# Performance work log

Hardware: AMD Instinct MI355X
Metric: run time of the kernel (lower is better)

The kernel has to match this reference:

```python
import jax, jax.numpy as jnp
import numpy as np

F_DIM, H, B, MAX = 128, 256, 256, 128
N = B * MAX            # 32768 nodes, 256 graphs of 128 nodes each
E = 524288             # avg degree 16
EPS = 1e-5


def _bn(x, g, b):
    # BatchNorm1d in training mode: biased batch stats over the node axis
    m = x.mean(0)
    v = x.var(0)
    return (x - m) * jax.lax.rsqrt(v + EPS) * g + b


def _gcn(x, W, b, src, dst, n):
    # PyG GCNConv: add self-loops, symmetric deg^-1/2 normalization
    h = x @ W
    loops = jnp.arange(n, dtype=src.dtype)
    s = jnp.concatenate([src, loops])
    d = jnp.concatenate([dst, loops])
    deg = jax.ops.segment_sum(jnp.ones_like(s, dtype=x.dtype), d, num_segments=n)
    dinv = jax.lax.rsqrt(jnp.maximum(deg, 1.0))
    norm = dinv[s] * dinv[d]
    out = jax.ops.segment_sum(h[s] * norm[:, None], d, num_segments=n)
    return out + b


def setup_inputs() -> dict:
    key = jax.random.key(0)
    ks = jax.random.split(key, 20)

    def xavier(k, shape, gain=1.414):
        lim = gain * np.sqrt(6.0 / (shape[0] + shape[1]))
        return jax.random.uniform(k, shape, jnp.float32, -lim, lim)

    inp = {}
    inp['x'] = jax.random.normal(ks[0], (N, F_DIM), jnp.float32)
    inp['src_local'] = jax.random.randint(ks[1], (E,), 0, MAX, jnp.int32)
    inp['dst_local'] = jax.random.randint(ks[2], (E,), 0, MAX, jnp.int32)
    dims = [(F_DIM, H), (H, H), (H, H)]
    for i, (di, do) in enumerate(dims):
        inp[f'gcn_w{i}'] = xavier(ks[3 + i], (di, do))
        inp[f'gcn_b{i}'] = jnp.zeros((do,), jnp.float32)
        inp[f'bn_g{i}'] = jnp.ones((do,), jnp.float32)
        inp[f'bn_b{i}'] = jnp.zeros((do,), jnp.float32)
    inp['sc_w0'] = xavier(ks[6], (F_DIM, H), 1.0)
    inp['sc_b0'] = jnp.zeros((H,), jnp.float32)
    inp['edge_w'] = xavier(ks[7], (H, H), 0.01)
    inp['fd_w0'] = xavier(ks[8], (H, H)); inp['fd_b0'] = jnp.zeros((H,), jnp.float32)
    inp['fd_g0'] = jnp.ones((H,), jnp.float32); inp['fd_be0'] = jnp.zeros((H,), jnp.float32)
    inp['fd_w1'] = xavier(ks[9], (H, H)); inp['fd_b1'] = jnp.zeros((H,), jnp.float32)
    inp['fd_g1'] = jnp.ones((H,), jnp.float32); inp['fd_be1'] = jnp.zeros((H,), jnp.float32)
    inp['fd_w2'] = xavier(ks[10], (H, F_DIM)); inp['fd_b2'] = jnp.zeros((F_DIM,), jnp.float32)
    inp['ph_w0'] = xavier(ks[11], (H, H)); inp['ph_b0'] = jnp.zeros((H,), jnp.float32)
    inp['ph_w1'] = xavier(ks[12], (H, H)); inp['ph_b1'] = jnp.zeros((H,), jnp.float32)
    return inp


def reference(x, src_local, dst_local,
              gcn_w0, gcn_b0, bn_g0, bn_b0, sc_w0, sc_b0,
              gcn_w1, gcn_b1, bn_g1, bn_b1,
              gcn_w2, gcn_b2, bn_g2, bn_b2,
              edge_w,
              fd_w0, fd_b0, fd_g0, fd_be0,
              fd_w1, fd_b1, fd_g1, fd_be1,
              fd_w2, fd_b2,
              ph_w0, ph_b0, ph_w1, ph_b1):
    n = x.shape[0]
    # global edge index: edge e belongs to graph e // (E//B); offset by g*MAX
    off = (jnp.arange(E, dtype=jnp.int32) // (E // B)) * MAX
    src = src_local + off
    dst = dst_local + off

    def block(h, W, b, g, bb, shortcut):
        res = shortcut(h)
        out = jax.nn.relu(_bn(_gcn(h, W, b, src, dst, n), g, bb))
        return jax.nn.relu(out + res)  # dropout is identity at inference

    z = block(x, gcn_w0, gcn_b0, bn_g0, bn_b0, lambda h: h @ sc_w0 + sc_b0)
    z = block(z, gcn_w1, gcn_b1, bn_g1, bn_b1, lambda h: h)
    z = block(z, gcn_w2, gcn_b2, bn_g2, bn_b2, lambda h: h)
    # F.normalize(p=2, dim=1)
    z = z / jnp.maximum(jnp.linalg.norm(z, axis=1, keepdims=True), 1e-12)

    # BilinearEdgeDecoder per graph, vectorized: sigmoid(Z W Z^T) with zero diag
    zb = z.reshape(B, MAX, H)
    adj = jax.nn.sigmoid(jnp.einsum('bnd,de,bme->bnm', zb, edge_w, zb))
    adj = adj * (1.0 - jnp.eye(MAX, dtype=adj.dtype))

    # Feature_Decoder: [Linear,ReLU,BN] x2 then Linear
    h = _bn(jax.nn.relu(z @ fd_w0 + fd_b0), fd_g0, fd_be0)
    h = _bn(jax.nn.relu(h @ fd_w1 + fd_b1), fd_g1, fd_be1)
    x_recon = h @ fd_w2 + fd_b2

    z_g = zb.max(axis=1)  # global_max_pool per graph
    z_g_mlp = jax.nn.relu(z_g @ ph_w0 + ph_b0) @ ph_w1 + ph_b1
    return (z, adj, x_recon, z_g, z_g_mlp)
```

## Files before the change

### kernel.cpp

```cpp
#include <hip/hip_runtime.h>
#include <hip/hip_bf16.h>

using bf = __hip_bfloat16;
typedef __attribute__((ext_vector_type(8))) short s8;
typedef __attribute__((ext_vector_type(4))) float f4;

constexpr int NN  = 32768;
constexpr int HD  = 256;

__device__ __forceinline__ float u2f(unsigned short h) {
    union { unsigned u; float f; } x; x.u = ((unsigned)h) << 16;
    return x.f;
}
__device__ __forceinline__ unsigned short f2u(float f) {
    union { float f; unsigned u; } x; x.f = f;
    unsigned r = x.u + 0x7FFF + ((x.u >> 16) & 1);
    return (unsigned short)(r >> 16);
}
__device__ __forceinline__ bf f2bf(float f) {
    unsigned short h = f2u(f);
    return *reinterpret_cast<bf*>(&h);
}
__device__ __forceinline__ float bf2f(bf b) {
    return u2f(*reinterpret_cast<unsigned short*>(&b));
}

__device__ __forceinline__ int swz(int row, int slot) {
    return row * 64 + ((slot ^ (row & 7)) << 3);
}
__device__ __forceinline__ int swz128(int row, int slot) {
    return row * 128 + ((slot ^ (row & 7)) << 3);
}

typedef const __attribute__((address_space(1))) unsigned int guint;
typedef __attribute__((address_space(3))) unsigned int luint;
__device__ __forceinline__ void gload16(const void* g, void* l) {
    __builtin_amdgcn_global_load_lds((guint*)g, (luint*)l, 16, 0, 0);
}

struct WTd { const float* src; int K, N, off; };
struct WTpack { WTd w[10]; };

__global__ __launch_bounds__(256) void k_prep(const int* __restrict__ srcL,
                                              const int* __restrict__ dstL,
                                              const float* __restrict__ xf,
                                              WTpack p, bf* __restrict__ A,
                                              bf* __restrict__ xb,
                                              bf* __restrict__ wT) {
    __shared__ __align__(16) float shm[8320];
    int b = blockIdx.x, t = threadIdx.x;
    if (b < 256) {
        float* sT = shm;
        float* sdin = shm + 8192;
        int g = b;
        const int* sg = srcL + (g << 11);
        const int* dg = dstL + (g << 11);
        if (t < 128) sdin[t] = 0.f;
        __syncthreads();
        for (int e = t; e < 2048; e += 256) atomicAdd(&sdin[dg[e]], 1.0f);
        __syncthreads();
        if (t < 128) sdin[t] = rsqrtf(sdin[t] + 1.0f);
        __syncthreads();
        bf* out = A + ((long)g << 14);
        for (int half = 0; half < 2; ++half) {
            for (int i = t; i < 8192; i += 256) sT[i] = 0.f;
            __syncthreads();
            for (int e = t; e < 2048; e += 256) {
                int s = sg[e], d = dg[e];
                if ((s >> 6) == half)
                    atomicAdd(&sT[(d << 6) + (s & 63)], sdin[s] * sdin[d]);
            }
            __syncthreads();
            if (t < 128 && (t >> 6) == half)
                sT[(t << 6) + (t & 63)] += sdin[t] * sdin[t];
            __syncthreads();
            for (int i4 = t; i4 < 2048; i4 += 256) {
                int d = i4 >> 4, c4 = (i4 & 15) * 4;
                float4 v = *(float4*)&sT[(d << 6) + c4];
                ushort4 u = make_ushort4(f2u(v.x), f2u(v.y), f2u(v.z), f2u(v.w));
                *(ushort4*)&out[(d << 7) + (half << 6) + c4] = u;
            }
            __syncthreads();
        }
    } else if (b < 416) {
        int idx = b - 256;
        WTd d = p.w[idx >> 4];
        int rem = idx & 15;
        int n0 = (rem & 3) * 64, k0 = (rem >> 2) * 64;
        if (n0 >= d.N || k0 >= d.K) return;
        float (*s)[65] = (float(*)[65])shm;
        int cc = t & 63, rq = t >> 6;
#pragma unroll
        for (int i = 0; i < 16; ++i) {
            int r = i * 4 + rq;
            s[r][cc] = d.src[(long)(k0 + r) * d.N + n0 + cc];
        }
        __syncthreads();
#pragma unroll
        for (int i = 0; i < 16; ++i) {
            int r = i * 4 + rq;
            wT[d.off + (long)(n0 + r) * d.K + k0 + cc] = f2bf(s[cc][r]);
        }
    } else {
        long base = (long)(b - 416) * 16384;
#pragma unroll
        for (int it = 0; it < 16; ++it) {
            long i4 = base + (it * 256 + t) * 4;
            float4 v = *(const float4*)&xf[i4];
            *(ushort4*)&xb[i4] = make_ushort4(f2u(v.x), f2u(v.y), f2u(v.z), f2u(v.w));
        }
    }
}

__device__ __forceinline__ void mfma_s1(const bf* sA, const bf* sB, f4 (&acc)[4][2],
                                        int wm, int wn, int l15, int kq) {
#pragma unroll
    for (int ks = 0; ks < 2; ++ks) {
        s8 af[4], bg[2];
#pragma unroll
        for (int f = 0; f < 4; ++f)
            af[f] = *(const s8*)&sA[swz(wm * 64 + f * 16 + l15, kq + 4 * ks)];
#pragma unroll
        for (int f = 0; f < 2; ++f)
            bg[f] = *(const s8*)&sB[swz(wn * 32 + f * 16 + l15, kq + 4 * ks)];
#pragma unroll
        for (int fr = 0; fr < 4; ++fr)
#pragma unroll
            for (int fc = 0; fc < 2; ++fc)
                acc[fr][fc] = __builtin_amdgcn_mfma_f32_16x16x32_bf16(
                    af[fr], bg[fc], acc[fr][fc], 0, 0, 0);
    }
}

__device__ __forceinline__ void mfma_s2(const bf* sA, const bf* sB, f4 (&acc)[4][2],
                                        int wm, int wn, int l15, int kq) {
#pragma unroll
    for (int ks = 0; ks < 4; ++ks) {
        s8 af[4], bg[2];
#pragma unroll
        for (int f = 0; f < 4; ++f)
            af[f] = *(const s8*)&sA[swz128(wm * 64 + f * 16 + l15, ks * 4 + kq)];
#pragma unroll
        for (int f = 0; f < 2; ++f)
            bg[f] = *(const s8*)&sB[swz128(wn * 32 + f * 16 + l15, ks * 4 + kq)];
#pragma unroll
        for (int fr = 0; fr < 4; ++fr)
#pragma unroll
            for (int fc = 0; fc < 2; ++fc)
                acc[fr][fc] = __builtin_amdgcn_mfma_f32_16x16x32_bf16(
                    af[fr], bg[fc], acc[fr][fc], 0, 0, 0);
    }
}

__device__ __forceinline__ void tstore(bf* sOut, f4 (&acc)[4][2],
                                       int wm, int wn, int l15, int kq) {
#pragma unroll
    for (int fr = 0; fr < 4; ++fr) {
        int rl = wm * 64 + fr * 16 + kq * 4;
#pragma unroll
        for (int fc = 0; fc < 2; ++fc) {
            int cl = wn * 32 + fc * 16 + l15;
            ushort4 q = make_ushort4(f2u(acc[fr][fc][0]), f2u(acc[fr][fc][1]),
                                     f2u(acc[fr][fc][2]), f2u(acc[fr][fc][3]));
            int off = cl * 128 + (((rl >> 3) ^ (cl & 7)) << 3) + (rl & 7);
            *(ushort4*)&sOut[off] = q;
        }
    }
}

template <int MODE>
__global__ __launch_bounds__(512) void k_fused(
    const bf* __restrict__ Xin,
    const bf* __restrict__ Res, const float* __restrict__ stats,
    const bf* __restrict__ Wt, const bf* __restrict__ Wt2,
    const float* __restrict__ scb, const bf* __restrict__ Adj,
    bf* __restrict__ Zout, bf* __restrict__ AG, bf* __restrict__ ResOut,
    float* __restrict__ part) {
    __shared__ __align__(16) bf sOut[16384];
    __shared__ __align__(16) bf sStg[16384];
    const int g = blockIdx.x;
    const int h = blockIdx.y;
    const int t = threadIdx.x;
    const int lane = t & 63, w = t >> 6;
    const int wm = w >> 2, wn = w & 3;
    const int l15 = lane & 15, kq = lane >> 4;
    constexpr int KS1 = (MODE == 2) ? 128 : 256;
    const bf* Xg = Xin + (long)g * ((MODE == 2) ? 16384 : 32768);
    const bf* Rg = (MODE == 0) ? Res + (long)g * 32768 : nullptr;

    f4 acc1[4][2] = {};
    for (int k0 = 0; k0 < KS1; k0 += 64) {
        __syncthreads();
#pragma unroll
        for (int i = 0; i < 2; ++i) {
            if constexpr (MODE == 0) {
                int sdx = i * 512 + t;
                int row = sdx >> 3, sl = sdx & 7;
                int c = k0 + sl * 8;
                s8 av = *(const s8*)&Xg[row * 256 + c];
                s8 rv = *(const s8*)&Rg[row * 256 + c];
                float4 sc0 = *(const float4*)&stats[c];
                float4 sc1 = *(const float4*)&stats[c + 4];
                float4 sh0 = *(const float4*)&stats[256 + c];
                float4 sh1 = *(const float4*)&stats[256 + c + 4];
                float scv[8] = {sc0.x, sc0.y, sc0.z, sc0.w, sc1.x, sc1.y, sc1.z, sc1.w};
                float shv[8] = {sh0.x, sh0.y, sh0.z, sh0.w, sh1.x, sh1.y, sh1.z, sh1.w};
                unsigned short* u = (unsigned short*)&av;
                const unsigned short* ru = (const unsigned short*)&rv;
#pragma unroll
                for (int j = 0; j < 8; ++j) {
                    float v = fmaf(u2f(u[j]), scv[j], shv[j]);
                    v = fmaxf(v, 0.f) + u2f(ru[j]);
                    u[j] = f2u(fmaxf(v, 0.f));
                }
                if (h == 0)
                    *(s8*)&Zout[(long)g * 32768 + row * 256 + c] = av;
                *(s8*)&sStg[swz(row, sl)] = av;
            } else {
                int r0 = i * 64 + 8 * w;
                int rw = r0 + (lane >> 3);
                int ps = ((lane & 7) ^ (rw & 7)) << 3;
                gload16(&Xg[rw * 128 + k0 + ps], &sStg[r0 * 64]);
            }
            {
                int r0 = i * 64 + 8 * w;
                int rw = r0 + (lane >> 3);
                int ps = ((lane & 7) ^ (rw & 7)) << 3;
                const bf* bsrc;
                if constexpr (MODE == 0)
                    bsrc = &Wt[(h * 128 + rw) * 256 + k0 + ps];
                else {
                    const bf* Wsrc = (h < 2) ? Wt : Wt2;
                    bsrc = &Wsrc[((h & 1) * 128 + rw) * 128 + k0 + ps];
                }
                gload16(bsrc, &sStg[8192 + r0 * 64]);
            }
        }
        __syncthreads();
        mfma_s1(sStg, sStg + 8192, acc1, wm, wn, l15, kq);
    }
    if (MODE == 2 && h >= 2) {
#pragma unroll
        for (int fr = 0; fr < 4; ++fr) {
            int rl = wm * 64 + fr * 16 + kq * 4;
#pragma unroll
            for (int fc = 0; fc < 2; ++fc) {
                int cl = wn * 32 + fc * 16 + l15;
                float bv = scb[(h - 2) * 128 + cl];
#pragma unroll
                for (int i = 0; i < 4; ++i)
                    ResOut[(long)(g * 128 + rl + i) * 256 + (h - 2) * 128 + cl] =
                        f2bf(acc1[fr][fc][i] + bv);
            }
        }
        return;
    }
    tstore(sOut, acc1, wm, wn, l15, kq);
    __syncthreads();
#pragma unroll
    for (int i = 0; i < 4; ++i) {
        int r0 = i * 32 + 4 * w;
        int rw = r0 + (lane >> 4);
        int ps = ((lane & 15) ^ (rw & 7)) << 3;
        gload16(&Adj[((long)g << 14) + rw * 128 + ps], &sStg[r0 * 128]);
    }
    __syncthreads();
    f4 acc2[4][2] = {};
    mfma_s2(sStg, sOut, acc2, wm, wn, l15, kq);
    float ps[2] = {0.f, 0.f}, ps2[2] = {0.f, 0.f};
#pragma unroll
    for (int fr = 0; fr < 4; ++fr) {
        int rl = wm * 64 + fr * 16 + kq * 4;
#pragma unroll
        for (int fc = 0; fc < 2; ++fc) {
            int cl = wn * 32 + fc * 16 + l15;
#pragma unroll
            for (int i = 0; i < 4; ++i) {
                float v = acc2[fr][fc][i];
                ps[fc] += v; ps2[fc] += v * v;
                AG[(long)(g * 128 + rl + i) * 256 + (h & 1) * 128 + cl] = f2bf(v);
            }
        }
    }
    __syncthreads();
    float* scr = (float*)sStg;
#pragma unroll
    for (int fc = 0; fc < 2; ++fc) {
        ps[fc] += __shfl_xor(ps[fc], 16);  ps[fc] += __shfl_xor(ps[fc], 32);
        ps2[fc] += __shfl_xor(ps2[fc], 16); ps2[fc] += __shfl_xor(ps2[fc], 32);
    }
    if (lane < 16) {
#pragma unroll
        for (int fc = 0; fc < 2; ++fc) {
            int c = wn * 32 + fc * 16 + lane;
            scr[(c * 2 + wm) * 2 + 0] = ps[fc];
            scr[(c * 2 + wm) * 2 + 1] = ps2[fc];
        }
    }
    __syncthreads();
    if (t < 256) {
        int col = t & 127, s = t >> 7;
        part[(long)((h & 1) * 256 + g) * 256 + s * 128 + col] =
            scr[(col * 2 + 0) * 2 + s] + scr[(col * 2 + 1) * 2 + s];
    }
}

__device__ __forceinline__ void fd_layer(const bf* Zg, const bf* W, const float* bias,
                                         bf* C, float* part, bf* sStg,
                                         int g, int h, int t, int lane,
                                         int wm, int wn, int l15, int kq) {
    f4 acc[4][2] = {};
    for (int k0 = 0; k0 < 256; k0 += 64) {
        __syncthreads();
#pragma unroll
        for (int i = 0; i < 2; ++i) {
            int sdx = i * 512 + t;
            int row = sdx >> 3, sl = sdx & 7;
            int c = k0 + sl * 8;
            *(s8*)&sStg[swz(row, sl)] = *(const s8*)&Zg[row * 256 + c];
            *(s8*)&sStg[8192 + swz(row, sl)] = *(const s8*)&W[(h * 128 + row) * 256 + c];
        }
        __syncthreads();
        mfma_s1(sStg, sStg + 8192, acc, wm, wn, l15, kq);
    }
    float ps[2] = {0.f, 0.f}, ps2[2] = {0.f, 0.f};
#pragma unroll
    for (int fr = 0; fr < 4; ++fr) {
        int rl = wm * 64 + fr * 16 + kq * 4;
#pragma unroll
        for (int fc = 0; fc < 2; ++fc) {
            int cl = wn * 32 + fc * 16 + l15;
            float bv = bias[h * 128 + cl];
#pragma unroll
            for (int i = 0; i < 4; ++i) {
                float v = fmaxf(acc[fr][fc][i] + bv, 0.f);
                ps[fc] += v; ps2[fc] += v * v;
                C[(long)(g * 128 + rl + i) * 256 + h * 128 + cl] = f2bf(v);
            }
        }
    }
    __syncthreads();
    float* scr = (float*)sStg;
#pragma unroll
    for (int fc = 0; fc < 2; ++fc) {
        ps[fc] += __shfl_xor(ps[fc], 16);  ps[fc] += __shfl_xor(ps[fc], 32);
        ps2[fc] += __shfl_xor(ps2[fc], 16); ps2[fc] += __shfl_xor(ps2[fc], 32);
    }
    if (lane < 16) {
#pragma unroll
        for (int fc = 0; fc < 2; ++fc) {
            int c = wn * 32 + fc * 16 + lane;
            scr[(c * 2 + wm) * 2 + 0] = ps[fc];
            scr[(c * 2 + wm) * 2 + 1] = ps2[fc];
        }
    }
    __syncthreads();
    if (t < 256) {
        int col = t & 127, s = t >> 7;
        part[(long)(h * 256 + g) * 256 + s * 128 + col] =
            scr[(col * 2 + 0) * 2 + s] + scr[(col * 2 + 1) * 2 + s];
    }
}

__global__ __launch_bounds__(512) void k_edfd(
    const bf* __restrict__ Zn, const bf* __restrict__ ewT,
    const bf* __restrict__ fdw, const float* __restrict__ fdb,
    const float* __restrict__ zgf, const bf* __restrict__ phw,
    const float* __restrict__ phb,
    float* __restrict__ adjout, bf* __restrict__ C, float* __restrict__ part,
    bf* __restrict__ P1b) {
    __shared__ __align__(16) bf sOut[16384];
    __shared__ __align__(16) bf sStg[16384];
    const int t = threadIdx.x;
    const int lane = t & 63, w = t >> 6;
    const int wm = w >> 2, wn = w & 3;
    const int l15 = lane & 15, kq = lane >> 4;
    if (blockIdx.x >= 768) {
        int bb = blockIdx.x - 768;
        int gz = bb & 1, h = bb >> 1;
        f4 acc[4][2] = {};
        for (int k0 = 0; k0 < 256; k0 += 64) {
            __syncthreads();
#pragma unroll
            for (int i = 0; i < 2; ++i) {
                int sdx = i * 512 + t;
                int row = sdx >> 3, sl = sdx & 7;
                int c = k0 + sl * 8;
                const float* src = zgf + (long)(gz * 128 + row) * 256 + c;
                float4 f0 = *(const float4*)src;
                float4 f1 = *(const float4*)(src + 4);
                unsigned short u[8] = {f2u(f0.x), f2u(f0.y), f2u(f0.z), f2u(f0.w),
                                       f2u(f1.x), f2u(f1.y), f2u(f1.z), f2u(f1.w)};
                *(s8*)&sStg[swz(row, sl)] = *(s8*)u;
                *(s8*)&sStg[8192 + swz(row, sl)] =
                    *(const s8*)&phw[(h * 128 + row) * 256 + c];
            }
            __syncthreads();
            mfma_s1(sStg, sStg + 8192, acc, wm, wn, l15, kq);
        }
#pragma unroll
        for (int fr = 0; fr < 4; ++fr) {
            int rl = wm * 64 + fr * 16 + kq * 4;
#pragma unroll
            for (int fc = 0; fc < 2; ++fc) {
                int cl = wn * 32 + fc * 16 + l15;
                float bv = phb[h * 128 + cl];
#pragma unroll
                for (int i = 0; i < 4; ++i)
                    P1b[(long)(gz * 128 + rl + i) * 256 + h * 128 + cl] =
                        f2bf(fmaxf(acc[fr][fc][i] + bv, 0.f));
            }
        }
        return;
    }
    if (blockIdx.x >= 256) {
        int bb = blockIdx.x - 256;
        int g = bb & 255, h = bb >> 8;
        fd_layer(Zn + (long)g * 32768, fdw, fdb, C, part, sStg,
                 g, h, t, lane, wm, wn, l15, kq);
        return;
    }
    const int g = blockIdx.x;
    const bf* Xg = Zn + (long)g * 32768;
    f4 acc2[4][2] = {};
    for (int h = 0; h < 2; ++h) {
        f4 acc1[4][2] = {};
        for (int k0 = 0; k0 < 256; k0 += 64) {
            __syncthreads();
#pragma unroll
            for (int i = 0; i < 2; ++i) {
                int sdx = i * 512 + t;
                int row = sdx >> 3, sl = sdx & 7;
                int c = k0 + sl * 8;
                *(s8*)&sStg[swz(row, sl)] = *(const s8*)&ewT[(h * 128 + row) * 256 + c];
                *(s8*)&sStg[8192 + swz(row, sl)] = *(const s8*)&Xg[row * 256 + c];
            }
            __syncthreads();
            mfma_s1(sStg, sStg + 8192, acc1, wm, wn, l15, kq);
        }
        tstore(sOut, acc1, wm, wn, l15, kq);
        __syncthreads();
#pragma unroll
        for (int i = 0; i < 4; ++i) {
            int sdx = i * 512 + t;
            int row = sdx >> 4, sl = sdx & 15;
            *(s8*)&sStg[swz128(row, sl)] = *(const s8*)&Xg[row * 256 + h * 128 + sl * 8];
        }
        __syncthreads();
        mfma_s2(sStg, sOut, acc2, wm, wn, l15, kq);
        __syncthreads();
    }
#pragma unroll
    for (int fr = 0; fr < 4; ++fr) {
        int rl = wm * 64 + fr * 16 + kq * 4;
#pragma unroll
        for (int fc = 0; fc < 2; ++fc) {
            int cl = wn * 32 + fc * 16 + l15;
            float vv[4];
#pragma unroll
            for (int i = 0; i < 4; ++i) {
                float v = 1.f / (1.f + __expf(-acc2[fr][fc][i]));
                if (cl == rl + i) v = 0.f;
                vv[i] = v;
            }
            float4 o; o.x = vv[0]; o.y = vv[1]; o.z = vv[2]; o.w = vv[3];
            *(float4*)&adjout[((long)g << 14) + cl * 128 + rl] = o;
        }
    }
}

template <int EPI, int OUT, bool PART, bool BNA, bool AF32>
__global__ __launch_bounds__(256) void mg(
    const void* __restrict__ Av, const bf* __restrict__ BT,
    const float* __restrict__ bias, const float* __restrict__ bnstats,
    float* __restrict__ Cf, bf* __restrict__ Cb, float* __restrict__ part,
    int M, int N, int K, int ldc) {
    __shared__ __align__(16) bf sAl[128 * 64];
    __shared__ __align__(16) bf sBl[128 * 64];
    const int m0 = blockIdx.y * 128, n0 = blockIdx.x * 128;
    const bf* Bb = BT + (long)n0 * K;
    const int t = threadIdx.x;
    const int lane = t & 63;
    const int w = t >> 6;
    const int wm = (w >> 1) * 64, wn = (w & 1) * 64;
    const int fr16 = lane & 15, kq = lane >> 4;
    f4 acc[4][4] = {};
    for (int k0 = 0; k0 < K; k0 += 64) {
#pragma unroll
        for (int i = 0; i < 4; ++i) {
            int sdx = i * 256 + t;
            int row = sdx >> 3, sl = sdx & 7;
            s8 av;
            if constexpr (AF32) {
                const float* src = (const float*)Av + (long)(m0 + row) * K + k0 + sl * 8;
                float4 f0 = *(const float4*)src;
                float4 f1 = *(const float4*)(src + 4);
                unsigned short u[8] = {f2u(f0.x), f2u(f0.y), f2u(f0.z), f2u(f0.w),
                                       f2u(f1.x), f2u(f1.y), f2u(f1.z), f2u(f1.w)};
                av = *(s8*)u;
            } else {
                av = *(const s8*)&((const bf*)Av)[(long)(m0 + row) * K + k0 + sl * 8];
                if constexpr (BNA) {
                    int c = k0 + sl * 8;
                    float4 sc0 = *(const float4*)&bnstats[c];
                    float4 sc1 = *(const float4*)&bnstats[c + 4];
                    float4 sh0 = *(const float4*)&bnstats[256 + c];
                    float4 sh1 = *(const float4*)&bnstats[256 + c + 4];
                    float scv[8] = {sc0.x, sc0.y, sc0.z, sc0.w, sc1.x, sc1.y, sc1.z, sc1.w};
                    float shv[8] = {sh0.x, sh0.y, sh0.z, sh0.w, sh1.x, sh1.y, sh1.z, sh1.w};
                    unsigned short* u = (unsigned short*)&av;
#pragma unroll
                    for (int j = 0; j < 8; ++j)
                        u[j] = f2u(fmaf(u2f(u[j]), scv[j], shv[j]));
                }
            }
            *(s8*)&sAl[swz(row, sl)] = av;
            *(s8*)&sBl[swz(row, sl)] = *(const s8*)&Bb[(long)row * K + k0 + sl * 8];
        }
        __syncthreads();
#pragma unroll
        for (int ks = 0; ks < 2; ++ks) {
            s8 af[4], bg[4];
#pragma unroll
            for (int f = 0; f < 4; ++f) {
                af[f] = *(const s8*)&sAl[swz(wm + f * 16 + fr16, kq + 4 * ks)];
                bg[f] = *(const s8*)&sBl[swz(wn + f * 16 + fr16, kq + 4 * ks)];
            }
#pragma unroll
            for (int fr = 0; fr < 4; ++fr)
#pragma unroll
                for (int fc = 0; fc < 4; ++fc)
                    acc[fr][fc] = __builtin_amdgcn_mfma_f32_16x16x32_bf16(
                        af[fr], bg[fc], acc[fr][fc], 0, 0, 0);
        }
        __syncthreads();
    }
    float ps[4], ps2[4];
    if (PART) {
#pragma unroll
        for (int fc = 0; fc < 4; ++fc) { ps[fc] = 0.f; ps2[fc] = 0.f; }
    }
#pragma unroll
    for (int fr = 0; fr < 4; ++fr) {
        int rl = wm + fr * 16 + (lane >> 4) * 4;
#pragma unroll
        for (int fc = 0; fc < 4; ++fc) {
            int cl = wn + fc * 16 + (lane & 15);
            int col = n0 + cl;
            float bv = bias[col];
#pragma unroll
            for (int i = 0; i < 4; ++i) {
                float v = acc[fr][fc][i] + bv;
                if (EPI == 2) v = fmaxf(v, 0.f);
                if (PART) { ps[fc] += v; ps2[fc] += v * v; }
                if (OUT == 0) Cf[(long)(m0 + rl + i) * ldc + col] = v;
                if (OUT == 1) Cb[(long)(m0 + rl + i) * ldc + col] = f2bf(v);
            }
        }
    }
    if (PART) {
        __syncthreads();
        float* scr = (float*)sAl;
#pragma unroll
        for (int fc = 0; fc < 4; ++fc) {
            ps[fc] += __shfl_xor(ps[fc], 16);  ps[fc] += __shfl_xor(ps[fc], 32);
            ps2[fc] += __shfl_xor(ps2[fc], 16); ps2[fc] += __shfl_xor(ps2[fc], 32);
        }
        if (lane < 16) {
#pragma unroll
            for (int fc = 0; fc < 4; ++fc) {
                scr[(w * 2 + 0) * 64 + fc * 16 + lane] = ps[fc];
                scr[(w * 2 + 1) * 64 + fc * 16 + lane] = ps2[fc];
            }
        }
        __syncthreads();
        int id = blockIdx.x * gridDim.y + blockIdx.y;
        int stat = t >> 7, c = t & 127;
        int ci = c & 63, half = c >> 6;
        float v = scr[(half * 2 + stat) * 64 + ci] + scr[((half + 2) * 2 + stat) * 64 + ci];
        part[(long)id * 256 + stat * 128 + c] = v;
    }
}

__global__ void k_bnfin(const float* __restrict__ part, const float* __restrict__ gam,
                        const float* __restrict__ bet, float* __restrict__ stats) {
    int ch = blockIdx.x;
    int half = ch >> 7, cc = ch & 127;
    int t = threadIdx.x;
    __shared__ float2 sm[256];
    const float* p = part + (long)(half * 256 + t) * 256;
    sm[t] = make_float2(p[cc], p[128 + cc]);
    __syncthreads();
    for (int s = 128; s > 0; s >>= 1) {
        if (t < s) { sm[t].x += sm[t + s].x; sm[t].y += sm[t + s].y; }
        __syncthreads();
    }
    if (t == 0) {
        float m = sm[0].x / (float)NN;
        float var = sm[0].y / (float)NN - m * m;
        float sc = rsqrtf(var + 1e-5f) * gam[ch];
        stats[ch]       = sc;
        stats[256 + ch] = bet[ch] - m * sc;
    }
}

__global__ __launch_bounds__(512) void k_finz(
    const bf* __restrict__ X, const float* __restrict__ stats,
    const bf* __restrict__ res, float* __restrict__ outz, bf* __restrict__ Znb,
    unsigned* __restrict__ zgu) {
    int g = blockIdx.x, half = blockIdx.y;
    int t = threadIdx.x;
    int lane = t & 63, w = t >> 6;
    int c4 = lane * 4;
    float4 sc = *(const float4*)&stats[c4];
    float4 sh = *(const float4*)&stats[256 + c4];
    float scv[4] = {sc.x, sc.y, sc.z, sc.w};
    float shv[4] = {sh.x, sh.y, sh.z, sh.w};
    float cmax[4] = {0.f, 0.f, 0.f, 0.f};
#pragma unroll
    for (int it = 0; it < 8; ++it) {
        int r = half * 64 + w * 8 + it;
        long i = (long)(g * 128 + r) * 256 + c4;
        ushort4 xv = *(const ushort4*)(X + i);
        ushort4 rv = *(const ushort4*)(res + i);
        unsigned short xs[4] = {xv.x, xv.y, xv.z, xv.w};
        unsigned short rs[4] = {rv.x, rv.y, rv.z, rv.w};
        float v[4];
        float s = 0.f;
#pragma unroll
        for (int j = 0; j < 4; ++j) {
            float vv = fmaf(u2f(xs[j]), scv[j], shv[j]);
            vv = fmaxf(vv, 0.f) + u2f(rs[j]);
            vv = fmaxf(vv, 0.f);
            v[j] = vv;
            s += vv * vv;
        }
#pragma unroll
        for (int o = 1; o < 64; o <<= 1) s += __shfl_xor(s, o);
        float den = fmaxf(sqrtf(s), 1e-12f);
        float4 fo;
        unsigned short us[4];
#pragma unroll
        for (int j = 0; j < 4; ++j) {
            float o = v[j] / den;
            ((float*)&fo)[j] = o;
            us[j] = f2u(o);
            cmax[j] = fmaxf(cmax[j], o);
        }
        *(float4*)(outz + i) = fo;
        *(ushort4*)(Znb + i) = make_ushort4(us[0], us[1], us[2], us[3]);
    }
    __shared__ float pm[8][256];
#pragma unroll
    for (int j = 0; j < 4; ++j) pm[w][c4 + j] = cmax[j];
    __syncthreads();
    if (t < 256) {
        float m = fmaxf(pm[0][t], pm[1][t]);
#pragma unroll
        for (int ww = 2; ww < 8; ++ww) m = fmaxf(m, pm[ww][t]);
        atomicMax(&zgu[g * 256 + t], __float_as_uint(m));
    }
}

template <int EPI, int OUT, bool PART, bool BNA, bool AF32>
static void MG(hipStream_t st, const void* A, const bf* BT, const float* bias,
               const float* bnstats, float* Cf, bf* Cb, float* part,
               int M, int N, int K, int ldc) {
    dim3 g(N / 128, M / 128, 1);
    mg<EPI, OUT, PART, BNA, AF32><<<g, 256, 0, st>>>(A, BT, bias, bnstats, Cf, Cb, part,
                                                     M, N, K, ldc);
}

extern "C" void kernel_launch(void* const* d_in, const int* in_sizes, int n_in,
                              void* d_out, int out_size, void* d_ws, size_t ws_size,
                              hipStream_t stream) {
    const float* x      = (const float*)d_in[0];
    const int*   srcL   = (const int*)d_in[1];
    const int*   dstL   = (const int*)d_in[2];
    const float* gcn_w0 = (const float*)d_in[3];
    const float* bn_g0  = (const float*)d_in[5];
    const float* bn_b0  = (const float*)d_in[6];
    const float* gcn_w1 = (const float*)d_in[7];
    const float* bn_g1  = (const float*)d_in[9];
    const float* bn_b1  = (const float*)d_in[10];
    const float* gcn_w2 = (const float*)d_in[11];
    const float* bn_g2  = (const float*)d_in[13];
    const float* bn_b2  = (const float*)d_in[14];
    const float* sc_w0  = (const float*)d_in[15];
    const float* sc_b0  = (const float*)d_in[16];
    const float* edge_w = (const float*)d_in[17];
    const float* fd_w0  = (const float*)d_in[18];
    const float* fd_b0  = (const float*)d_in[19];
    const float* fd_g0  = (const float*)d_in[20];
    const float* fd_be0 = (const float*)d_in[21];
    const float* fd_w1  = (const float*)d_in[22];
    const float* fd_b1  = (const float*)d_in[23];
    const float* fd_g1  = (const float*)d_in[24];
    const float* fd_be1 = (const float*)d_in[25];
    const float* fd_w2  = (const float*)d_in[26];
    const float* fd_b2  = (const float*)d_in[27];
    const float* ph_w0  = (const float*)d_in[28];
    const float* ph_b0  = (const float*)d_in[29];
    const float* ph_w1  = (const float*)d_in[30];
    const float* ph_b1  = (const float*)d_in[31];

    float* out     = (float*)d_out;
    float* out_z   = out;
    float* out_adj = out + 8388608;
    float* out_xr  = out + 12582912;
    float* out_zg  = out + 16777216;
    float* out_zgm = out + 16842752;

    float* w     = (float*)d_ws;
    float* part  = w;
    float* stats = w + 131072;
    bf*    wT    = (bf*)(w + 131584);
    bf*    Aadjb = (bf*)(w + 410112);
    bf*    U4    = (bf*)(w + 2507264);
    bf*    U1    = (bf*)(w + 6701568);
    bf*    U2    = (bf*)(w + 10895872);
    bf*    U3    = (bf*)(w + 15090176);
    bf*    P1b   = (bf*)(w + 19284480);
    bf*    xb    = (bf*)(w + 19317248);

    WTpack pk;
    pk.w[0] = {gcn_w0, 128, 256, 0};
    pk.w[1] = {sc_w0,  128, 256, 32768};
    pk.w[2] = {gcn_w1, 256, 256, 65536};
    pk.w[3] = {gcn_w2, 256, 256, 131072};
    pk.w[4] = {edge_w, 256, 256, 196608};
    pk.w[5] = {fd_w0,  256, 256, 262144};
    pk.w[6] = {fd_w1,  256, 256, 327680};
    pk.w[7] = {fd_w2,  256, 128, 393216};
    pk.w[8] = {ph_w0,  256, 256, 425984};
    pk.w[9] = {ph_w1,  256, 256, 491520};

    hipMemsetAsync(out_zg, 0, 65536 * 4, stream);

    k_prep<<<672, 256, 0, stream>>>(srcL, dstL, x, pk, Aadjb, xb, wT);

    k_fused<2><<<dim3(256, 4), 512, 0, stream>>>(xb, nullptr, nullptr,
                                                 wT + 0, wT + 32768, sc_b0, Aadjb,
                                                 nullptr, U2, U1, part);
    k_bnfin<<<256, 256, 0, stream>>>(part, bn_g0, bn_b0, stats);

    k_fused<0><<<dim3(256, 2), 512, 0, stream>>>(U2, U1, stats,
                                                 wT + 65536, nullptr, nullptr, Aadjb,
                                                 U3, U4, nullptr, part);
    k_bnfin<<<256, 256, 0, stream>>>(part, bn_g1, bn_b1, stats);

    k_fused<0><<<dim3(256, 2), 512, 0, stream>>>(U4, U3, stats,
                                                 wT + 131072, nullptr, nullptr, Aadjb,
                                                 U1, U2, nullptr, part);
    k_bnfin<<<256, 256, 0, stream>>>(part, bn_g2, bn_b2, stats);

    k_finz<<<dim3(256, 2), 512, 0, stream>>>(U2, stats, U1, out_z, U3,
                                             (unsigned*)out_zg);

    k_edfd<<<772, 512, 0, stream>>>(U3, wT + 196608, wT + 262144, fd_b0,
                                    out_zg, wT + 425984, ph_b0,
                                    out_adj, U4, part, P1b);
    k_bnfin<<<256, 256, 0, stream>>>(part, fd_g0, fd_be0, stats);

    MG<2, 1, true, true, false>(stream, U4, wT + 327680, fd_b1, stats,
                                nullptr, U2, part, NN, HD, HD, 256);
    k_bnfin<<<256, 256, 0, stream>>>(part, fd_g1, fd_be1, stats);
    MG<1, 0, false, true, false>(stream, U2, wT + 393216, fd_b2, stats,
                                 out_xr, nullptr, nullptr, NN, 128, HD, 128);

    MG<1, 0, false, false, false>(stream, P1b, wT + 491520, ph_b1, nullptr,
                                  out_zgm, nullptr, nullptr, 256, 256, 256, 256);
}
```

Measured before the change: 177.9 us.

## Double-buffer stage-1 GEMM staging through sOut to overlap loads with MFMA

The stage-1 K loop now prefetches the next 64-wide K slice of inputs and weights into the alternate LDS buffer (sOut/sStg ping-pong) while the MFMAs consume the current one. This drops one barrier per iteration and hides global-load latency behind compute. The tstore and Adj tiles swap buffers, which removes one more barrier. The cost is more live registers during the MODE 0 elementwise prefetch, and correctness relies on gload16 completing before the end-of-iteration barrier.

```diff
diff --git a/kernel.cpp b/kernel.cpp
--- a/kernel.cpp
+++ b/kernel.cpp
@@ -164,6 +164,58 @@
                                      f2u(acc[fr][fc][2]), f2u(acc[fr][fc][3]));
             int off = cl * 128 + (((rl >> 3) ^ (cl & 7)) << 3) + (rl & 7);
             *(ushort4*)&sOut[off] = q;
+        }
+    }
+}
+
+template <int MODE>
+__device__ __forceinline__ void stg1(const bf* Xg, const bf* Rg,
+                                     const float* stats, const bf* Wt,
+                                     const bf* Wt2, bf* Zout, bf* dst,
+                                     int g, int h, int k0, int t, int lane, int w) {
+#pragma unroll
+    for (int i = 0; i < 2; ++i) {
+        if constexpr (MODE == 0) {
+            int sdx = i * 512 + t;
+            int row = sdx >> 3, sl = sdx & 7;
+            int c = k0 + sl * 8;
+            s8 av = *(const s8*)&Xg[row * 256 + c];
+            s8 rv = *(const s8*)&Rg[row * 256 + c];
+            float4 sc0 = *(const float4*)&stats[c];
+            float4 sc1 = *(const float4*)&stats[c + 4];
+            float4 sh0 = *(const float4*)&stats[256 + c];
+            float4 sh1 = *(const float4*)&stats[256 + c + 4];
+            float scv[8] = {sc0.x, sc0.y, sc0.z, sc0.w, sc1.x, sc1.y, sc1.z, sc1.w};
+            float shv[8] = {sh0.x, sh0.y, sh0.z, sh0.w, sh1.x, sh1.y, sh1.z, sh1.w};
+            unsigned short* u = (unsigned short*)&av;
+            const unsigned short* ru = (const unsigned short*)&rv;
+#pragma unroll
+            for (int j = 0; j < 8; ++j) {
+                float v = fmaf(u2f(u[j]), scv[j], shv[j]);
+                v = fmaxf(v, 0.f) + u2f(ru[j]);
+                u[j] = f2u(fmaxf(v, 0.f));
+            }
+            if (h == 0)
+                *(s8*)&Zout[(long)g * 32768 + row * 256 + c] = av;
+            *(s8*)&dst[swz(row, sl)] = av;
+        } else {
+            int r0 = i * 64 + 8 * w;
+            int rw = r0 + (lane >> 3);
+            int ps = ((lane & 7) ^ (rw & 7)) << 3;
+            gload16(&Xg[rw * 128 + k0 + ps], &dst[r0 * 64]);
+        }
+        {
+            int r0 = i * 64 + 8 * w;
+            int rw = r0 + (lane >> 3);
+            int ps = ((lane & 7) ^ (rw & 7)) << 3;
+            const bf* bsrc;
+            if constexpr (MODE == 0)
+                bsrc = &Wt[(h * 128 + rw) * 256 + k0 + ps];
+            else {
+                const bf* Wsrc = (h < 2) ? Wt : Wt2;
+                bsrc = &Wsrc[((h & 1) * 128 + rw) * 128 + k0 + ps];
+            }
+            gload16(bsrc, &dst[8192 + r0 * 64]);
         }
     }
 }
@@ -185,59 +237,21 @@
     const int wm = w >> 2, wn = w & 3;
     const int l15 = lane & 15, kq = lane >> 4;
     constexpr int KS1 = (MODE == 2) ? 128 : 256;
+    constexpr int NK = KS1 / 64;
     const bf* Xg = Xin + (long)g * ((MODE == 2) ? 16384 : 32768);
     const bf* Rg = (MODE == 0) ? Res + (long)g * 32768 : nullptr;
 
     f4 acc1[4][2] = {};
-    for (int k0 = 0; k0 < KS1; k0 += 64) {
-        __syncthreads();
-#pragma unroll
-        for (int i = 0; i < 2; ++i) {
-            if constexpr (MODE == 0) {
-                int sdx = i * 512 + t;
-                int row = sdx >> 3, sl = sdx & 7;
-                int c = k0 + sl * 8;
-                s8 av = *(const s8*)&Xg[row * 256 + c];
-                s8 rv = *(const s8*)&Rg[row * 256 + c];
-                float4 sc0 = *(const float4*)&stats[c];
-                float4 sc1 = *(const float4*)&stats[c + 4];
-                float4 sh0 = *(const float4*)&stats[256 + c];
-                float4 sh1 = *(const float4*)&stats[256 + c + 4];
-                float scv[8] = {sc0.x, sc0.y, sc0.z, sc0.w, sc1.x, sc1.y, sc1.z, sc1.w};
-                float shv[8] = {sh0.x, sh0.y, sh0.z, sh0.w, sh1.x, sh1.y, sh1.z, sh1.w};
-                unsigned short* u = (unsigned short*)&av;
-                const unsigned short* ru = (const unsigned short*)&rv;
-#pragma unroll
-                for (int j = 0; j < 8; ++j) {
-                    float v = fmaf(u2f(u[j]), scv[j], shv[j]);
-                    v = fmaxf(v, 0.f) + u2f(ru[j]);
-                    u[j] = f2u(fmaxf(v, 0.f));
-                }
-                if (h == 0)
-                    *(s8*)&Zout[(long)g * 32768 + row * 256 + c] = av;
-                *(s8*)&sStg[swz(row, sl)] = av;
-            } else {
-                int r0 = i * 64 + 8 * w;
-                int rw = r0 + (lane >> 3);
-                int ps = ((lane & 7) ^ (rw & 7)) << 3;
-                gload16(&Xg[rw * 128 + k0 + ps], &sStg[r0 * 64]);
-            }
-            {
-                int r0 = i * 64 + 8 * w;
-                int rw = r0 + (lane >> 3);
-                int ps = ((lane & 7) ^ (rw & 7)) << 3;
-                const bf* bsrc;
-                if constexpr (MODE == 0)
-                    bsrc = &Wt[(h * 128 + rw) * 256 + k0 + ps];
-                else {
-                    const bf* Wsrc = (h < 2) ? Wt : Wt2;
-                    bsrc = &Wsrc[((h & 1) * 128 + rw) * 128 + k0 + ps];
-                }
-                gload16(bsrc, &sStg[8192 + r0 * 64]);
-            }
-        }
-        __syncthreads();
-        mfma_s1(sStg, sStg + 8192, acc1, wm, wn, l15, kq);
+    stg1<MODE>(Xg, Rg, stats, Wt, Wt2, Zout, sStg, g, h, 0, t, lane, w);
+    __syncthreads();
+#pragma unroll
+    for (int k = 0; k < NK; ++k) {
+        bf* cur = (k & 1) ? sOut : sStg;
+        if (k + 1 < NK)
+            stg1<MODE>(Xg, Rg, stats, Wt, Wt2, Zout, (k & 1) ? sStg : sOut,
+                       g, h, (k + 1) * 64, t, lane, w);
+        mfma_s1(cur, cur + 8192, acc1, wm, wn, l15, kq);
+        __syncthreads();
     }
     if (MODE == 2 && h >= 2) {
 #pragma unroll
@@ -255,18 +269,17 @@
         }
         return;
     }
-    tstore(sOut, acc1, wm, wn, l15, kq);
-    __syncthreads();
+    tstore(sStg, acc1, wm, wn, l15, kq);
 #pragma unroll
     for (int i = 0; i < 4; ++i) {
         int r0 = i * 32 + 4 * w;
         int rw = r0 + (lane >> 4);
         int ps = ((lane & 15) ^ (rw & 7)) << 3;
-        gload16(&Adj[((long)g << 14) + rw * 128 + ps], &sStg[r0 * 128]);
+        gload16(&Adj[((long)g << 14) + rw * 128 + ps], &sOut[r0 * 128]);
     }
     __syncthreads();
     f4 acc2[4][2] = {};
-    mfma_s2(sStg, sOut, acc2, wm, wn, l15, kq);
+    mfma_s2(sOut, sStg, acc2, wm, wn, l15, kq);
     float ps[2] = {0.f, 0.f}, ps2[2] = {0.f, 0.f};
 #pragma unroll
     for (int fr = 0; fr < 4; ++fr) {
```

Measured after the change: 175.5 us. Within noise of the previous version (-1.4%).
